# Performance work log

Measured on AMD Instinct MI355X. Metric: run time of the kernel, lower is better.

Reference implementation:

```python
import jax, jax.numpy as jnp
import numpy as np

D_MODEL = 1024
H = 16          # n_heads (kv heads)
G = 2           # n_gqa_groups
DQ = 64         # d_queries
DV = 64         # d_values
MAXLEN = 2048
NSEG = 8
SEG = MAXLEN // NSEG  # 256
EPS = 1e-5
ROPE_THETA = 10000.0


def setup_inputs() -> dict:
    key = jax.random.key(0)
    ks = jax.random.split(key, 10)
    N = 8
    w = lambda k, sh: jax.random.normal(k, sh, dtype=jnp.float32) * 0.02
    return {
        "query_sequences": jax.random.normal(ks[0], (N, MAXLEN, D_MODEL), dtype=jnp.float32),
        "key_sequences": jax.random.normal(ks[1], (N, MAXLEN, D_MODEL), dtype=jnp.float32),
        "value_sequences": jax.random.normal(ks[2], (N, MAXLEN, D_MODEL), dtype=jnp.float32),
        "ln_w": jnp.ones((D_MODEL,), dtype=jnp.float32),
        "ln_b": jnp.zeros((D_MODEL,), dtype=jnp.float32),
        "Wq": w(ks[3], (G * H * DQ, D_MODEL)),
        "Wk": w(ks[4], (H * DQ, D_MODEL)),
        "Wv": w(ks[5], (H * DV, D_MODEL)),
        "Wo": w(ks[6], (D_MODEL, H * DV)),
        "Wkc": w(ks[7], (DQ, SEG * DQ)),
        "bkc": jnp.zeros((DQ,), dtype=jnp.float32),
        "Wvc": w(ks[8], (DV, SEG * DV)),
        "bvc": jnp.zeros((DV,), dtype=jnp.float32),
    }


def _layernorm(x, w, b):
    mu = x.mean(-1, keepdims=True)
    var = ((x - mu) ** 2).mean(-1, keepdims=True)
    return (x - mu) * jax.lax.rsqrt(var + EPS) * w + b


def _rope(x):
    # x: [..., seq, DQ]; full-dim interleaved RoPE (rotary-embedding-torch convention)
    seq = x.shape[-2]
    inv_freq = 1.0 / (ROPE_THETA ** (jnp.arange(0, DQ, 2, dtype=jnp.float32) / DQ))  # [DQ/2]
    ang = jnp.arange(seq, dtype=jnp.float32)[:, None] * inv_freq[None, :]            # [seq, DQ/2]
    ang = jnp.repeat(ang, 2, axis=-1)                                                # [seq, DQ]
    cos, sin = jnp.cos(ang), jnp.sin(ang)
    x2 = x.reshape(x.shape[:-1] + (DQ // 2, 2))
    xrot = jnp.stack([-x2[..., 1], x2[..., 0]], axis=-1).reshape(x.shape)
    return x * cos + xrot * sin


def _forward(query_sequences, key_sequences, value_sequences,
             ln_w, ln_b, Wq, Wk, Wv, Wo, Wkc, bkc, Wvc, bvc):
    N, t, _ = query_sequences.shape
    q = _layernorm(query_sequences, ln_w, ln_b)
    k = _layernorm(key_sequences, ln_w, ln_b)
    v = _layernorm(value_sequences, ln_w, ln_b)

    qh = (q @ Wq.T).reshape(N, t, G, H, DQ).transpose(0, 2, 3, 1, 4)  # [N,G,H,t,DQ]
    kh = (k @ Wk.T).reshape(N, t, H, DQ).transpose(0, 2, 1, 3)        # [N,H,T,DQ]
    vh = (v @ Wv.T).reshape(N, t, H, DV).transpose(0, 2, 1, 3)        # [N,H,T,DV]

    qh = _rope(qh)
    kh = _rope(kh)

    # split into NSEG segments along time; keep last 2 raw, compress the rest
    kseg = kh.reshape(N, H, NSEG, SEG, DQ)
    vseg = vh.reshape(N, H, NSEG, SEG, DV)
    recent_k = kseg[:, :, -2:].reshape(N, H, 2 * SEG, DQ)
    recent_v = vseg[:, :, -2:].reshape(N, H, 2 * SEG, DV)
    k_sum = jax.nn.elu(kseg[:, :, :-2].reshape(N, H, NSEG - 2, SEG * DQ) @ Wkc.T + bkc)  # [N,H,S-2,DQ]
    v_sum = jax.nn.elu(vseg[:, :, :-2].reshape(N, H, NSEG - 2, SEG * DV) @ Wvc.T + bvc)
    K = jnp.concatenate([k_sum, recent_k], axis=-2)  # [N,H,Tk,DQ], Tk = (NSEG-2) + 2*SEG
    V = jnp.concatenate([v_sum, recent_v], axis=-2)

    # NOTE: original einsum sums over the GQA group axis g
    attn = jnp.einsum('nghtq,nhTq->nhtT', qh, K) * (1.0 / DQ ** 0.5)
    attn = 30.0 * jnp.tanh(attn / 30.0)  # grok scaled attn

    Tk = K.shape[-2]
    causal = jnp.arange(Tk)[None, :] <= jnp.arange(t)[:, None]  # tril slice [t, Tk]
    attn = jnp.where(causal, attn, -jnp.inf)
    attn = jax.nn.softmax(attn, axis=-1)

    out = jnp.einsum('nhtT,nhTv->nhtv', attn, V)
    out = out.transpose(0, 2, 1, 3).reshape(N, t, H * DV)
    return out @ Wo.T


def reference(query_sequences, key_sequences, value_sequences,
              ln_w, ln_b, Wq, Wk, Wv, Wo, Wkc, bkc, Wvc, bvc):
    return _forward(query_sequences, key_sequences, value_sequences,
                    ln_w, ln_b, Wq, Wk, Wv, Wo, Wkc, bkc, Wvc, bvc)
```

## Files before the change

### kernel.cpp

```cpp
#include <hip/hip_runtime.h>
#include <stdint.h>

#define DEV static __device__ __forceinline__

typedef unsigned short u16;
typedef unsigned int u32;
typedef __attribute__((ext_vector_type(4))) float f32x4;
typedef __attribute__((ext_vector_type(8))) short bf16x8;

DEV float bf2f(u16 u) { u32 x = ((u32)u) << 16; float f; __builtin_memcpy(&f, &x, 4); return f; }
DEV u16 f2bf(float f) { u32 x; __builtin_memcpy(&x, &f, 4); x = x + 0x7fffu + ((x >> 16) & 1u); return (u16)(x >> 16); }
DEV float lo16(u32 p) { u32 x = p << 16; float f; __builtin_memcpy(&f, &x, 4); return f; }
DEV float hi16(u32 p) { u32 x = p & 0xffff0000u; float f; __builtin_memcpy(&f, &x, 4); return f; }
DEV u32 pack2(float a, float b) { return (u32)f2bf(a) | ((u32)f2bf(b) << 16); }

DEV u32 cvtpk(float lo, float hi) {
  u32 r; asm("v_cvt_pk_bf16_f32 %0, %1, %2" : "=v"(r) : "v"(lo), "v"(hi)); return r;
}
DEV bf16x8 pk8(f32x4 a, f32x4 b) {
  union { u32 u[4]; bf16x8 v; } x;
  x.u[0] = cvtpk(a[0], a[1]); x.u[1] = cvtpk(a[2], a[3]);
  x.u[2] = cvtpk(b[0], b[1]); x.u[3] = cvtpk(b[2], b[3]);
  return x.v;
}

DEV f32x4 mfma16(bf16x8 a, bf16x8 b, f32x4 c) {
  return __builtin_amdgcn_mfma_f32_16x16x32_bf16(a, b, c, 0, 0, 0);
}

DEV void gl_lds16(const u16* g, u16* l) {
  __builtin_amdgcn_global_load_lds((const __attribute__((address_space(1))) void*)g,
                                   (__attribute__((address_space(3))) void*)l, 16, 0, 0);
}

__global__ __launch_bounds__(256) void prep_wqe_kernel(const float* __restrict__ Wq, u16* __restrict__ out) {
  int id = blockIdx.x * 256 + threadIdx.x;
  float4 a = ((const float4*)Wq)[id];
  float4 b = ((const float4*)Wq)[id + 262144];
  ushort4 o; o.x = f2bf(a.x + b.x); o.y = f2bf(a.y + b.y); o.z = f2bf(a.z + b.z); o.w = f2bf(a.w + b.w);
  ((ushort4*)out)[id] = o;
}

__global__ __launch_bounds__(256) void cast_w_kernel(const float* __restrict__ src, u16* __restrict__ dst) {
  int id = blockIdx.x * 256 + threadIdx.x;
  float4 a = ((const float4*)src)[id];
  ushort4 o; o.x = f2bf(a.x); o.y = f2bf(a.y); o.z = f2bf(a.z); o.w = f2bf(a.w);
  ((ushort4*)dst)[id] = o;
}

__global__ __launch_bounds__(256) void rope_table_kernel(float* __restrict__ ct, float* __restrict__ st) {
  int id = blockIdx.x * 256 + threadIdx.x;
  int t = id >> 5, i = id & 31;
  double ang = (double)t * pow(10000.0, -(double)(2 * i) / 64.0);
  ct[id] = (float)cos(ang);
  st[id] = (float)sin(ang);
}

__global__ __launch_bounds__(256) void ln_kernel(const float* __restrict__ x, const float* __restrict__ w,
                                                 const float* __restrict__ b, u16* __restrict__ out) {
  int row = blockIdx.x, t = threadIdx.x;
  float4 v = ((const float4*)(x + (size_t)row * 1024))[t];
  float s = v.x + v.y + v.z + v.w;
  float s2 = v.x * v.x + v.y * v.y + v.z * v.z + v.w * v.w;
#pragma unroll
  for (int off = 32; off; off >>= 1) { s += __shfl_xor(s, off, 64); s2 += __shfl_xor(s2, off, 64); }
  __shared__ float red[8];
  if ((t & 63) == 0) { red[t >> 6] = s; red[4 + (t >> 6)] = s2; }
  __syncthreads();
  s = red[0] + red[1] + red[2] + red[3];
  s2 = red[4] + red[5] + red[6] + red[7];
  float mu = s * 0.0009765625f;
  float var = s2 * 0.0009765625f - mu * mu;
  float rstd = rsqrtf(var + 1e-5f);
  float4 wv = ((const float4*)w)[t];
  float4 bv = ((const float4*)b)[t];
  ushort4 o;
  o.x = f2bf((v.x - mu) * rstd * wv.x + bv.x);
  o.y = f2bf((v.y - mu) * rstd * wv.y + bv.y);
  o.z = f2bf((v.z - mu) * rstd * wv.z + bv.z);
  o.w = f2bf((v.w - mu) * rstd * wv.w + bv.w);
  *(ushort4*)(out + (size_t)row * 1024 + t * 4) = o;
}

template <int OUTF32>
__global__ __launch_bounds__(256, 2) void gemm_nt(const u16* __restrict__ A, const u16* __restrict__ B,
                                                  void* __restrict__ Cout, int M, int Nd, int K) {
  __shared__ u16 As[4096], Bs[4096];
  int tid = threadIdx.x, lane = tid & 63, wv = tid >> 6;
  int l15 = lane & 15, lq = lane >> 4;
  int bm = blockIdx.x * 128, bn = blockIdx.y * 128;
  int wm = (wv >> 1) * 64, wn = (wv & 1) * 64;
  f32x4 acc[4][4] = {};
  for (int k0 = 0; k0 < K; k0 += 32) {
    __syncthreads();
#pragma unroll
    for (int it = 0; it < 2; ++it) {
      int ia = wv * 2 + it;
      int row = ia * 16 + (lane >> 2);
      int qs = lane & 3;
      int qg = qs ^ (row & 3);
      gl_lds16(A + (size_t)(bm + row) * K + k0 + qg * 8, &As[ia * 512]);
      gl_lds16(B + (size_t)(bn + row) * K + k0 + qg * 8, &Bs[ia * 512]);
    }
    __syncthreads();
    bf16x8 af[4], bfr[4];
#pragma unroll
    for (int mt = 0; mt < 4; ++mt) {
      int r = wm + mt * 16 + l15;
      af[mt] = *(const bf16x8*)&As[r * 32 + ((lq ^ (r & 3)) * 8)];
    }
#pragma unroll
    for (int nt = 0; nt < 4; ++nt) {
      int r = wn + nt * 16 + l15;
      bfr[nt] = *(const bf16x8*)&Bs[r * 32 + ((lq ^ (r & 3)) * 8)];
    }
#pragma unroll
    for (int mt = 0; mt < 4; ++mt)
#pragma unroll
      for (int nt = 0; nt < 4; ++nt)
        acc[mt][nt] = mfma16(af[mt], bfr[nt], acc[mt][nt]);
  }
#pragma unroll
  for (int mt = 0; mt < 4; ++mt)
#pragma unroll
    for (int nt = 0; nt < 4; ++nt)
#pragma unroll
      for (int i = 0; i < 4; ++i) {
        int row = bm + wm + mt * 16 + lq * 4 + i;
        int col = bn + wn + nt * 16 + l15;
        if (OUTF32) ((float*)Cout)[(size_t)row * Nd + col] = acc[mt][nt][i];
        else ((u16*)Cout)[(size_t)row * Nd + col] = f2bf(acc[mt][nt][i]);
      }
}

__global__ __launch_bounds__(256) void rope_kernel(u16* __restrict__ qc, u16* __restrict__ kh,
                                                   const float* __restrict__ ct, const float* __restrict__ st) {
  u32 id = blockIdx.x * 256 + threadIdx.x;
  u16* base = qc;
  if (id >= 2097152u) { base = kh; id -= 2097152u; }
  size_t e0 = (size_t)id * 8;
  int row = (int)(e0 >> 10);
  int col = (int)(e0 & 1023);
  int t = row & 2047;
  int i0 = (col & 63) >> 1;
  float4 c = *(const float4*)(ct + t * 32 + i0);
  float4 s = *(const float4*)(st + t * 32 + i0);
  uint4 u = *(const uint4*)(base + e0);
  float x0 = lo16(u.x), x1 = hi16(u.x), x2 = lo16(u.y), x3 = hi16(u.y);
  float x4 = lo16(u.z), x5 = hi16(u.z), x6 = lo16(u.w), x7 = hi16(u.w);
  uint4 o;
  o.x = pack2(x0 * c.x - x1 * s.x, x1 * c.x + x0 * s.x);
  o.y = pack2(x2 * c.y - x3 * s.y, x3 * c.y + x2 * s.y);
  o.z = pack2(x4 * c.z - x5 * s.z, x5 * c.z + x4 * s.z);
  o.w = pack2(x6 * c.w - x7 * s.w, x7 * c.w + x6 * s.w);
  *(uint4*)(base + e0) = o;
}

__global__ __launch_bounds__(512) void compress_partial_kernel(
    const u16* __restrict__ kh, const u16* __restrict__ vh,
    const u16* __restrict__ wkcb, const u16* __restrict__ wvcb,
    float* __restrict__ part) {
  int mt = blockIdx.x, ksl = blockIdx.y, kv = blockIdx.z;
  const u16* src = kv ? vh : kh;
  const u16* W = kv ? wvcb : wkcb;
  int tid = threadIdx.x, lane = tid & 63, wv = tid >> 6;
  int l15 = lane & 15, lq = lane >> 4;
  int r = mt * 16 + l15;
  int nh = r / 6, s = r % 6;
  int n = nh >> 4, h = nh & 15;
  const u16* arow = src + ((size_t)(n * 2048 + s * 256)) * 1024 + h * 64;
  f32x4 acc[4] = {};
  int kbase = (ksl * 8 + wv) * 256;
#pragma unroll
  for (int ks = 0; ks < 8; ++ks) {
    int k0 = kbase + ks * 32;
    int tau = k0 >> 6, d0 = k0 & 63;
    bf16x8 a = *(const bf16x8*)(arow + (size_t)tau * 1024 + d0 + lq * 8);
#pragma unroll
    for (int nt = 0; nt < 4; ++nt) {
      bf16x8 b = *(const bf16x8*)(W + (size_t)(nt * 16 + l15) * 16384 + k0 + lq * 8);
      acc[nt] = mfma16(a, b, acc[nt]);
    }
  }
  __shared__ float red[8][16][68];
#pragma unroll
  for (int nt = 0; nt < 4; ++nt)
#pragma unroll
    for (int i = 0; i < 4; ++i)
      red[wv][lq * 4 + i][nt * 16 + l15] = acc[nt][i];
  __syncthreads();
  int row = tid >> 5, o0 = (tid & 31) * 2;
  float v0 = 0.f, v1 = 0.f;
#pragma unroll
  for (int w8 = 0; w8 < 8; ++w8) { v0 += red[w8][row][o0]; v1 += red[w8][row][o0 + 1]; }
  size_t base = ((size_t)(kv * 8 + ksl) * 768 + mt * 16 + row) * 64 + o0;
  part[base] = v0;
  part[base + 1] = v1;
}

__global__ __launch_bounds__(256) void compress_finalize_kernel(
    const float* __restrict__ part, const float* __restrict__ bkc, const float* __restrict__ bvc,
    u16* __restrict__ kp, u16* __restrict__ vtp) {
  int id = blockIdx.x * 256 + threadIdx.x;
  int kv = blockIdx.y;
  int r = id >> 6, o = id & 63;
  float v = kv ? bvc[o] : bkc[o];
#pragma unroll
  for (int s8 = 0; s8 < 8; ++s8) v += part[((size_t)(kv * 8 + s8) * 768 + r) * 64 + o];
  v = v > 0.f ? v : expm1f(v);
  int nh = r / 6, s = r % 6;
  if (kv) vtp[((size_t)nh * 64 + o) * 576 + s] = f2bf(v);
  else    kp[((size_t)nh * 576 + s) * 64 + o] = f2bf(v);
}

__global__ __launch_bounds__(256) void copy_recent_kernel(const u16* __restrict__ kh, const u16* __restrict__ vh,
                                                          u16* __restrict__ kp, u16* __restrict__ vtp) {
  int bid = blockIdx.x;
  if (bid < 2280) {
    int u = bid * 256 + threadIdx.x;
    int dq8 = u & 7; int rest = u >> 3; int Tm6 = rest % 570; int nh = rest / 570;
    if (nh >= 128) return;
    uint4 val = {0, 0, 0, 0};
    if (Tm6 < 512) {
      int n = nh >> 4, h = nh & 15;
      val = *(const uint4*)&kh[((size_t)(n * 2048 + 1536 + Tm6)) * 1024 + h * 64 + dq8 * 8];
    }
    *(uint4*)&kp[((size_t)nh * 576 + 6 + Tm6) * 64 + dq8 * 8] = val;
  } else {
    int u = (bid - 2280) * 256 + threadIdx.x;
    int d = u & 63; int rest = u >> 6; int tch = rest % 72; int nh = rest / 72;
    if (nh >= 128) return;
    int n = nh >> 4, h = nh & 15;
#pragma unroll
    for (int ii = 0; ii < 8; ++ii) {
      int T = tch * 8 + ii;
      if (T < 6) continue;
      u16 v = 0;
      if (T < 518) v = vh[((size_t)(n * 2048 + 1536 + (T - 6))) * 1024 + h * 64 + d];
      vtp[((size_t)nh * 64 + d) * 576 + T] = v;
    }
  }
}

__global__ __launch_bounds__(256) void attn_kernel(const u16* __restrict__ qc, const u16* __restrict__ Kp,
                                                   const u16* __restrict__ VTp, u16* __restrict__ ao) {
  int qt = blockIdx.x, h = blockIdx.y, n = blockIdx.z;
  int tid = threadIdx.x, lane = tid & 63, wv = tid >> 6;
  int l15 = lane & 15, lq = lane >> 4;
  __shared__ u16 KS[4096], VS[4096];
  __shared__ float PS[4][1088];
  int q0 = qt * 64 + wv * 16;
  const u16* qrowp = qc + ((size_t)(n * 2048 + q0 + l15)) * 1024 + h * 64;
  bf16x8 aq0 = *(const bf16x8*)(qrowp + lq * 8);
  bf16x8 aq1 = *(const bf16x8*)(qrowp + 32 + lq * 8);
  const u16* Kph = Kp + (size_t)(n * 16 + h) * 576 * 64;
  const u16* Vph = VTp + (size_t)(n * 16 + h) * 64 * 576;
  f32x4 oa[4] = {};
  float rs[4] = {0.f, 0.f, 0.f, 0.f};
  float* PSW = &PS[wv][0];
  const float C1 = 0.012022458674074693f;
  const float C2 = -86.56170245333781f;
  int nchunks = min(qt + 1, 9);
  for (int tc = 0; tc < nchunks; ++tc) {
    int Tbase = tc * 64;
    __syncthreads();
#pragma unroll
    for (int it = 0; it < 2; ++it) {
      int slot = it * 256 + tid;
      int row = slot >> 3, qq = slot & 7;
      int sw = (qq ^ (row & 7)) * 8;
      *(uint4*)&KS[row * 64 + sw] = *(const uint4*)&Kph[(size_t)(Tbase + row) * 64 + qq * 8];
      *(uint4*)&VS[row * 64 + sw] = *(const uint4*)&Vph[(size_t)row * 576 + Tbase + qq * 8];
    }
    __syncthreads();
    f32x4 sv[4];
    __builtin_amdgcn_s_setprio(1);
#pragma unroll
    for (int tt = 0; tt < 4; ++tt) {
      int row = tt * 16 + l15, r7 = row & 7;
      bf16x8 b0 = *(const bf16x8*)&KS[row * 64 + ((lq ^ r7) * 8)];
      bf16x8 b1 = *(const bf16x8*)&KS[row * 64 + (((4 | lq) ^ r7) * 8)];
      f32x4 c = {0.f, 0.f, 0.f, 0.f};
      c = mfma16(aq0, b0, c);
      c = mfma16(aq1, b1, c);
      sv[tt] = c;
    }
    __builtin_amdgcn_s_setprio(0);
    float p[4][4];
    bool needmask = (tc == qt) || (tc == 8);
    if (needmask) {
      int qb = q0 + lq * 4;
#pragma unroll
      for (int tt = 0; tt < 4; ++tt) {
        int T = Tbase + tt * 16 + l15;
        bool tval = (T < 518);
#pragma unroll
        for (int i = 0; i < 4; ++i) {
          float e = __builtin_amdgcn_exp2f(sv[tt][i] * C1);
          float pe = __builtin_amdgcn_exp2f(C2 * __builtin_amdgcn_rcpf(e + 1.f));
          bool ok = tval && (T <= qb + i);
          pe = ok ? pe : 0.f;
          p[tt][i] = pe;
          rs[i] += pe;
        }
      }
    } else {
#pragma unroll
      for (int tt = 0; tt < 4; ++tt)
#pragma unroll
        for (int i = 0; i < 4; ++i) {
          float e = __builtin_amdgcn_exp2f(sv[tt][i] * C1);
          float pe = __builtin_amdgcn_exp2f(C2 * __builtin_amdgcn_rcpf(e + 1.f));
          p[tt][i] = pe;
          rs[i] += pe;
        }
    }
#pragma unroll
    for (int tt = 0; tt < 4; ++tt)
#pragma unroll
      for (int i = 0; i < 4; ++i)
        PSW[(lq * 4 + i) * 68 + tt * 16 + l15] = p[tt][i];
    const float* prow = PSW + l15 * 68;
    f32x4 r0a = *(const f32x4*)(prow + lq * 8);
    f32x4 r0b = *(const f32x4*)(prow + lq * 8 + 4);
    f32x4 r1a = *(const f32x4*)(prow + lq * 8 + 32);
    f32x4 r1b = *(const f32x4*)(prow + lq * 8 + 36);
    bf16x8 pa0 = pk8(r0a, r0b);
    bf16x8 pa1 = pk8(r1a, r1b);
    __builtin_amdgcn_s_setprio(1);
#pragma unroll
    for (int ct = 0; ct < 4; ++ct) {
      int row = ct * 16 + l15, r7 = row & 7;
      bf16x8 bv0 = *(const bf16x8*)&VS[row * 64 + ((lq ^ r7) * 8)];
      bf16x8 bv1 = *(const bf16x8*)&VS[row * 64 + (((4 | lq) ^ r7) * 8)];
      oa[ct] = mfma16(pa0, bv0, oa[ct]);
      oa[ct] = mfma16(pa1, bv1, oa[ct]);
    }
    __builtin_amdgcn_s_setprio(0);
  }
#pragma unroll
  for (int i = 0; i < 4; ++i)
#pragma unroll
    for (int off = 1; off < 16; off <<= 1) rs[i] += __shfl_xor(rs[i], off, 64);
  u16* aop = ao + ((size_t)(n * 2048)) * 1024 + h * 64;
#pragma unroll
  for (int i = 0; i < 4; ++i) {
    float inv = 1.0f / rs[i];
    int q = q0 + lq * 4 + i;
#pragma unroll
    for (int ct = 0; ct < 4; ++ct) {
      int dv = ct * 16 + l15;
      aop[(size_t)q * 1024 + dv] = f2bf(oa[ct][i] * inv);
    }
  }
}

extern "C" void kernel_launch(void* const* d_in, const int* in_sizes, int n_in,
                              void* d_out, int out_size, void* d_ws, size_t ws_size,
                              hipStream_t stream) {
  const float* q_in = (const float*)d_in[0];
  const float* k_in = (const float*)d_in[1];
  const float* v_in = (const float*)d_in[2];
  const float* ln_w = (const float*)d_in[3];
  const float* ln_b = (const float*)d_in[4];
  const float* Wq = (const float*)d_in[5];
  const float* Wk = (const float*)d_in[6];
  const float* Wv = (const float*)d_in[7];
  const float* Wo = (const float*)d_in[8];
  const float* Wkc = (const float*)d_in[9];
  const float* bkc = (const float*)d_in[10];
  const float* Wvc = (const float*)d_in[11];
  const float* bvc = (const float*)d_in[12];

  char* ws = (char*)d_ws;
  const size_t MB = 1u << 20;
  u16* wqe = (u16*)(ws + 0 * MB);
  u16* wkb = (u16*)(ws + 2 * MB);
  u16* wvb = (u16*)(ws + 4 * MB);
  u16* wob = (u16*)(ws + 6 * MB);
  u16* wkcb = (u16*)(ws + 8 * MB);
  u16* wvcb = (u16*)(ws + 10 * MB);
  float* cost = (float*)(ws + 12 * MB);
  float* sint = (float*)(ws + 12 * MB + 262144);
  u16* xn = (u16*)(ws + 13 * MB);
  float* partf = (float*)(ws + 13 * MB);
  u16* qcb = (u16*)(ws + 45 * MB);
  u16* khb = (u16*)(ws + 77 * MB);
  u16* vhb = (u16*)(ws + 109 * MB);
  u16* kp = (u16*)(ws + 141 * MB);
  u16* vtp = (u16*)(ws + 141 * MB + 9437184);
  u16* aob = khb;

  prep_wqe_kernel<<<1024, 256, 0, stream>>>(Wq, wqe);
  cast_w_kernel<<<1024, 256, 0, stream>>>(Wk, wkb);
  cast_w_kernel<<<1024, 256, 0, stream>>>(Wv, wvb);
  cast_w_kernel<<<1024, 256, 0, stream>>>(Wo, wob);
  cast_w_kernel<<<1024, 256, 0, stream>>>(Wkc, wkcb);
  cast_w_kernel<<<1024, 256, 0, stream>>>(Wvc, wvcb);
  rope_table_kernel<<<256, 256, 0, stream>>>(cost, sint);

  dim3 gg(128, 8);
  ln_kernel<<<16384, 256, 0, stream>>>(q_in, ln_w, ln_b, xn);
  gemm_nt<0><<<gg, 256, 0, stream>>>(xn, wqe, qcb, 16384, 1024, 1024);
  ln_kernel<<<16384, 256, 0, stream>>>(k_in, ln_w, ln_b, xn);
  gemm_nt<0><<<gg, 256, 0, stream>>>(xn, wkb, khb, 16384, 1024, 1024);
  ln_kernel<<<16384, 256, 0, stream>>>(v_in, ln_w, ln_b, xn);
  gemm_nt<0><<<gg, 256, 0, stream>>>(xn, wvb, vhb, 16384, 1024, 1024);

  rope_kernel<<<16384, 256, 0, stream>>>(qcb, khb, cost, sint);
  compress_partial_kernel<<<dim3(48, 8, 2), 512, 0, stream>>>(khb, vhb, wkcb, wvcb, partf);
  compress_finalize_kernel<<<dim3(192, 2), 256, 0, stream>>>(partf, bkc, bvc, kp, vtp);
  copy_recent_kernel<<<4584, 256, 0, stream>>>(khb, vhb, kp, vtp);
  attn_kernel<<<dim3(32, 16, 8), 256, 0, stream>>>(qcb, kp, vtp, aob);
  gemm_nt<1><<<gg, 256, 0, stream>>>(aob, wob, (float*)d_out, 16384, 1024, 1024);
}
```

Baseline: 445.4 us.

## Fuse RoPE into projection GEMM epilogue and register-prefetch attention K/V tiles

Removes the standalone RoPE pass by applying the rotation in the Q and K projection GEMM epilogues. Each lane gets its rotation partner through a lane shuffle and reads cos/sin from a new interleaved table. This saves a full read-modify-write pass over the Q and K activations. Separately, the attention kernel now loads the next chunk's K/V tiles into registers while the current chunk is being computed, overlapping global loads with MFMA work at the cost of extra registers.

New measurement: 435.1 us. 2.3% less time.

```diff
diff --git a/kernel.cpp b/kernel.cpp
--- a/kernel.cpp
+++ b/kernel.cpp
@@ -48,12 +48,12 @@
   ((ushort4*)dst)[id] = o;
 }
 
-__global__ __launch_bounds__(256) void rope_table_kernel(float* __restrict__ ct, float* __restrict__ st) {
+__global__ __launch_bounds__(256) void rope_cs_kernel(float* __restrict__ cs) {
   int id = blockIdx.x * 256 + threadIdx.x;
   int t = id >> 5, i = id & 31;
   double ang = (double)t * pow(10000.0, -(double)(2 * i) / 64.0);
-  ct[id] = (float)cos(ang);
-  st[id] = (float)sin(ang);
+  cs[id * 2] = (float)cos(ang);
+  cs[id * 2 + 1] = (float)sin(ang);
 }
 
 __global__ __launch_bounds__(256) void ln_kernel(const float* __restrict__ x, const float* __restrict__ w,
@@ -82,9 +82,10 @@
   *(ushort4*)(out + (size_t)row * 1024 + t * 4) = o;
 }
 
-template <int OUTF32>
+template <int MODE>
 __global__ __launch_bounds__(256, 2) void gemm_nt(const u16* __restrict__ A, const u16* __restrict__ B,
-                                                  void* __restrict__ Cout, int M, int Nd, int K) {
+                                                  void* __restrict__ Cout, int M, int Nd, int K,
+                                                  const float* __restrict__ cs) {
   __shared__ u16 As[4096], Bs[4096];
   int tid = threadIdx.x, lane = tid & 63, wv = tid >> 6;
   int l15 = lane & 15, lq = lane >> 4;
@@ -128,32 +129,20 @@
       for (int i = 0; i < 4; ++i) {
         int row = bm + wm + mt * 16 + lq * 4 + i;
         int col = bn + wn + nt * 16 + l15;
-        if (OUTF32) ((float*)Cout)[(size_t)row * Nd + col] = acc[mt][nt][i];
-        else ((u16*)Cout)[(size_t)row * Nd + col] = f2bf(acc[mt][nt][i]);
+        float x = acc[mt][nt][i];
+        if (MODE == 1) {
+          ((float*)Cout)[(size_t)row * Nd + col] = x;
+        } else if (MODE == 0) {
+          ((u16*)Cout)[(size_t)row * Nd + col] = f2bf(x);
+        } else {
+          float xp = __shfl_xor(x, 1, 64);
+          int t = row & 2047;
+          int i0 = (col & 63) >> 1;
+          float2 csv = *(const float2*)(cs + ((size_t)t * 32 + i0) * 2);
+          float r = (col & 1) ? (x * csv.x + xp * csv.y) : (x * csv.x - xp * csv.y);
+          ((u16*)Cout)[(size_t)row * Nd + col] = f2bf(r);
+        }
       }
-}
-
-__global__ __launch_bounds__(256) void rope_kernel(u16* __restrict__ qc, u16* __restrict__ kh,
-                                                   const float* __restrict__ ct, const float* __restrict__ st) {
-  u32 id = blockIdx.x * 256 + threadIdx.x;
-  u16* base = qc;
-  if (id >= 2097152u) { base = kh; id -= 2097152u; }
-  size_t e0 = (size_t)id * 8;
-  int row = (int)(e0 >> 10);
-  int col = (int)(e0 & 1023);
-  int t = row & 2047;
-  int i0 = (col & 63) >> 1;
-  float4 c = *(const float4*)(ct + t * 32 + i0);
-  float4 s = *(const float4*)(st + t * 32 + i0);
-  uint4 u = *(const uint4*)(base + e0);
-  float x0 = lo16(u.x), x1 = hi16(u.x), x2 = lo16(u.y), x3 = hi16(u.y);
-  float x4 = lo16(u.z), x5 = hi16(u.z), x6 = lo16(u.w), x7 = hi16(u.w);
-  uint4 o;
-  o.x = pack2(x0 * c.x - x1 * s.x, x1 * c.x + x0 * s.x);
-  o.y = pack2(x2 * c.y - x3 * s.y, x3 * c.y + x2 * s.y);
-  o.z = pack2(x4 * c.z - x5 * s.z, x5 * c.z + x4 * s.z);
-  o.w = pack2(x6 * c.w - x7 * s.w, x7 * c.w + x6 * s.w);
-  *(uint4*)(base + e0) = o;
 }
 
 __global__ __launch_bounds__(512) void compress_partial_kernel(
@@ -261,16 +250,29 @@
   const float C1 = 0.012022458674074693f;
   const float C2 = -86.56170245333781f;
   int nchunks = min(qt + 1, 9);
+  int srow0 = tid >> 3, sq0 = tid & 7;
+  int srow1 = (256 + tid) >> 3, sq1 = tid & 7;
+  int ksw0 = srow0 * 64 + ((sq0 ^ (srow0 & 7)) * 8);
+  int ksw1 = srow1 * 64 + ((sq1 ^ (srow1 & 7)) * 8);
+  uint4 kr0, kr1, vr0, vr1;
+  {
+    kr0 = *(const uint4*)&Kph[(size_t)srow0 * 64 + sq0 * 8];
+    kr1 = *(const uint4*)&Kph[(size_t)srow1 * 64 + sq1 * 8];
+    vr0 = *(const uint4*)&Vph[(size_t)srow0 * 576 + sq0 * 8];
+    vr1 = *(const uint4*)&Vph[(size_t)srow1 * 576 + sq1 * 8];
+  }
   for (int tc = 0; tc < nchunks; ++tc) {
-    int Tbase = tc * 64;
     __syncthreads();
-#pragma unroll
-    for (int it = 0; it < 2; ++it) {
-      int slot = it * 256 + tid;
-      int row = slot >> 3, qq = slot & 7;
-      int sw = (qq ^ (row & 7)) * 8;
-      *(uint4*)&KS[row * 64 + sw] = *(const uint4*)&Kph[(size_t)(Tbase + row) * 64 + qq * 8];
-      *(uint4*)&VS[row * 64 + sw] = *(const uint4*)&Vph[(size_t)row * 576 + Tbase + qq * 8];
+    *(uint4*)&KS[ksw0] = kr0;
+    *(uint4*)&KS[ksw1] = kr1;
+    *(uint4*)&VS[ksw0] = vr0;
+    *(uint4*)&VS[ksw1] = vr1;
+    if (tc + 1 < nchunks) {
+      int Tb = (tc + 1) * 64;
+      kr0 = *(const uint4*)&Kph[(size_t)(Tb + srow0) * 64 + sq0 * 8];
+      kr1 = *(const uint4*)&Kph[(size_t)(Tb + srow1) * 64 + sq1 * 8];
+      vr0 = *(const uint4*)&Vph[(size_t)srow0 * 576 + Tb + sq0 * 8];
+      vr1 = *(const uint4*)&Vph[(size_t)srow1 * 576 + Tb + sq1 * 8];
     }
     __syncthreads();
     f32x4 sv[4];
@@ -290,6 +292,7 @@
     bool needmask = (tc == qt) || (tc == 8);
     if (needmask) {
       int qb = q0 + lq * 4;
+      int Tbase = tc * 64;
 #pragma unroll
       for (int tt = 0; tt < 4; ++tt) {
         int T = Tbase + tt * 16 + l15;
@@ -380,8 +383,7 @@
   u16* wob = (u16*)(ws + 6 * MB);
   u16* wkcb = (u16*)(ws + 8 * MB);
   u16* wvcb = (u16*)(ws + 10 * MB);
-  float* cost = (float*)(ws + 12 * MB);
-  float* sint = (float*)(ws + 12 * MB + 262144);
+  float* csb = (float*)(ws + 12 * MB);
   u16* xn = (u16*)(ws + 13 * MB);
   float* partf = (float*)(ws + 13 * MB);
   u16* qcb = (u16*)(ws + 45 * MB);
@@ -397,20 +399,19 @@
   cast_w_kernel<<<1024, 256, 0, stream>>>(Wo, wob);
   cast_w_kernel<<<1024, 256, 0, stream>>>(Wkc, wkcb);
   cast_w_kernel<<<1024, 256, 0, stream>>>(Wvc, wvcb);
-  rope_table_kernel<<<256, 256, 0, stream>>>(cost, sint);
+  rope_cs_kernel<<<256, 256, 0, stream>>>(csb);
 
   dim3 gg(128, 8);
   ln_kernel<<<16384, 256, 0, stream>>>(q_in, ln_w, ln_b, xn);
-  gemm_nt<0><<<gg, 256, 0, stream>>>(xn, wqe, qcb, 16384, 1024, 1024);
+  gemm_nt<2><<<gg, 256, 0, stream>>>(xn, wqe, qcb, 16384, 1024, 1024, csb);
   ln_kernel<<<16384, 256, 0, stream>>>(k_in, ln_w, ln_b, xn);
-  gemm_nt<0><<<gg, 256, 0, stream>>>(xn, wkb, khb, 16384, 1024, 1024);
+  gemm_nt<2><<<gg, 256, 0, stream>>>(xn, wkb, khb, 16384, 1024, 1024, csb);
   ln_kernel<<<16384, 256, 0, stream>>>(v_in, ln_w, ln_b, xn);
-  gemm_nt<0><<<gg, 256, 0, stream>>>(xn, wvb, vhb, 16384, 1024, 1024);
-
-  rope_kernel<<<16384, 256, 0, stream>>>(qcb, khb, cost, sint);
+  gemm_nt<0><<<gg, 256, 0, stream>>>(xn, wvb, vhb, 16384, 1024, 1024, csb);
+
   compress_partial_kernel<<<dim3(48, 8, 2), 512, 0, stream>>>(khb, vhb, wkcb, wvcb, partf);
   compress_finalize_kernel<<<dim3(192, 2), 256, 0, stream>>>(partf, bkc, bvc, kp, vtp);
   copy_recent_kernel<<<4584, 256, 0, stream>>>(khb, vhb, kp, vtp);
   attn_kernel<<<dim3(32, 16, 8), 256, 0, stream>>>(qcb, kp, vtp, aob);
-  gemm_nt<1><<<gg, 256, 0, stream>>>(aob, wob, (float*)d_out, 16384, 1024, 1024);
-}
+  gemm_nt<1><<<gg, 256, 0, stream>>>(aob, wob, (float*)d_out, 16384, 1024, 1024, csb);
+}
```
